# Kernel tuning notes

Hardware: AMD Instinct MI355X
Metric: run time of the kernel (lower is better)

Reference implementation:

```python
import jax, jax.numpy as jnp
import numpy as np

# dims
N, T, DIN = 256, 32, 2048      # batch, time, gpt output dim
H = 2048                        # MLP hidden
G, C, D = 2, 16, 256            # vq groups, codebook size, code dim
W, A = 5, 7                     # action window, action dim
WA = W * A                      # output_size
DEC_H = 512                     # vqvae decoder hidden
NT = N * T


def _mk(key, shape, scale=0.02):
    return jax.random.normal(key, shape, dtype=jnp.float32) * scale


def setup_inputs() -> dict:
    key = jax.random.key(0)
    ks = jax.random.split(key, 16)
    inp = {
        "x": jax.random.normal(ks[0], (N, T, DIN), dtype=jnp.float32),
        # bin1 MLP: DIN -> H -> H -> C
        "w11": _mk(ks[1], (DIN, H)), "b11": jnp.zeros((H,), jnp.float32),
        "w12": _mk(ks[2], (H, H)),   "b12": jnp.zeros((H,), jnp.float32),
        "w13": _mk(ks[3], (H, C)),   "b13": jnp.zeros((C,), jnp.float32),
        # bin2 MLP: DIN+C -> H -> C
        "w21": _mk(ks[4], (DIN + C, H)), "b21": jnp.zeros((H,), jnp.float32),
        "w22": _mk(ks[5], (H, C)),       "b22": jnp.zeros((C,), jnp.float32),
        # offset MLP: DIN -> H -> H -> G*C*WA
        "wo1": _mk(ks[6], (DIN, H)), "bo1": jnp.zeros((H,), jnp.float32),
        "wo2": _mk(ks[7], (H, H)),   "bo2": jnp.zeros((H,), jnp.float32),
        "wo3": _mk(ks[8], (H, G * C * WA)), "bo3": jnp.zeros((G * C * WA,), jnp.float32),
        # residual-VQ codebooks: (G, C, D)
        "codebook": _mk(ks[9], (G, C, D), scale=1.0),
        # frozen vqvae decoder: G*D -> DEC_H -> WA
        "wd1": _mk(ks[10], (G * D, DEC_H)), "bd1": jnp.zeros((DEC_H,), jnp.float32),
        "wd2": _mk(ks[11], (DEC_H, WA)),    "bd2": jnp.zeros((WA,), jnp.float32),
    }
    return inp


def reference(x, w11, b11, w12, b12, w13, b13, w21, b21, w22, b22,
              wo1, bo1, wo2, bo2, wo3, bo3, codebook, wd1, bd1, wd2, bd2):
    xf = x.reshape(NT, DIN)
    # bin1 logits
    h = jax.nn.relu(xf @ w11 + b11)
    h = jax.nn.relu(h @ w12 + b12)
    cbet_logits1 = h @ w13 + b13                       # (NT, C)
    # offsets
    o = jax.nn.relu(xf @ wo1 + bo1)
    o = jax.nn.relu(o @ wo2 + bo2)
    cbet_offsets = (o @ wo3 + bo3).reshape(NT, G, C, WA)
    # multinomial sampling (== categorical over softmax(logits))
    key = jax.random.key(42)
    k1, k2 = jax.random.split(key)
    s1 = jax.random.categorical(k1, cbet_logits1)      # (NT,)
    one_hot1 = jax.nn.one_hot(s1, C, dtype=xf.dtype)
    h2 = jax.nn.relu(jnp.concatenate([xf, one_hot1], axis=1) @ w21 + b21)
    cbet_logits2 = h2 @ w22 + b22                      # (NT, C)
    s2 = jax.random.categorical(k2, cbet_logits2)
    sampled_centers = jnp.stack([s1, s2], axis=1)      # (NT, G)
    # gather offsets at sampled codes, sum over groups
    nt_idx = jnp.arange(NT)[:, None]
    g_idx = jnp.arange(G)[None, :]
    sampled_offsets = cbet_offsets[nt_idx, g_idx, sampled_centers].sum(axis=1)  # (NT, WA)
    # vq codebook lookup + frozen decoder (detached in torch)
    centers = codebook[g_idx, sampled_centers]          # (NT, G, D)
    dec_in = jax.lax.stop_gradient(centers.reshape(NT, G * D))
    decoded = jax.nn.relu(dec_in @ wd1 + bd1) @ wd2 + bd2
    decoded = jax.lax.stop_gradient(decoded)            # (NT, WA)
    predicted = (decoded.reshape(NT, W, A) + sampled_offsets.reshape(NT, W, A))
    predicted_action = predicted.reshape(N, T, WA)
    return predicted_action, decoded, cbet_logits1, cbet_logits2, sampled_centers
```

## Files before the change

kernel.cpp:

```cpp
#include <hip/hip_runtime.h>
#include <cstdint>
#include <cstddef>

#define NT_   8192
#define DIN_  2048
#define H_    2048
#define C_    16
#define G_    2
#define D_    256
#define WA_   35
#define DECH_ 512
#define NPAD_ 1152

typedef _Float16 f16;
typedef _Float16 h4 __attribute__((ext_vector_type(4)));
typedef _Float16 h8 __attribute__((ext_vector_type(8)));
typedef float fx4 __attribute__((ext_vector_type(4)));

typedef __attribute__((address_space(1))) const void gvoid_t;
typedef __attribute__((address_space(3))) void lvoid_t;

__device__ __forceinline__ void gld16(const void* g, void* l) {
  __builtin_amdgcn_global_load_lds((gvoid_t*)(uintptr_t)g,
                                   (lvoid_t*)(uint32_t)(uintptr_t)l, 16, 0, 0);
}

__device__ __forceinline__ void barrier_() {
  asm volatile("" ::: "memory");
  __builtin_amdgcn_s_barrier();
  asm volatile("" ::: "memory");
}

template <int N>
__device__ __forceinline__ void waitvm() {
  if constexpr (N == 8)      asm volatile("s_waitcnt vmcnt(8)" ::: "memory");
  else if constexpr (N == 6) asm volatile("s_waitcnt vmcnt(6)" ::: "memory");
  else if constexpr (N == 2) asm volatile("s_waitcnt vmcnt(2)" ::: "memory");
  else                       asm volatile("s_waitcnt vmcnt(0)" ::: "memory");
}

#define MFMA_(d, a, b) d = __builtin_amdgcn_mfma_f32_16x16x32_f16(a, b, d, 0, 0, 0)

__host__ __device__ inline void tf2x32(uint32_t k0, uint32_t k1,
                                       uint32_t x0, uint32_t x1,
                                       uint32_t& o0, uint32_t& o1) {
  const uint32_t ks2 = k0 ^ k1 ^ 0x1BD11BDAu;
  uint32_t ks[3] = {k0, k1, ks2};
  x0 += ks[0]; x1 += ks[1];
  const uint32_t R0[4] = {13u, 15u, 26u, 6u};
  const uint32_t R1[4] = {17u, 29u, 16u, 24u};
#pragma unroll
  for (int g = 0; g < 5; ++g) {
    const uint32_t* R = (g & 1) ? R1 : R0;
#pragma unroll
    for (int r = 0; r < 4; ++r) {
      x0 += x1;
      x1 = (x1 << R[r]) | (x1 >> (32u - R[r]));
      x1 ^= x0;
    }
    x0 += ks[(g + 1) % 3];
    x1 += ks[(g + 2) % 3] + (uint32_t)(g + 1);
  }
  o0 = x0; o1 = x1;
}

__global__ __launch_bounds__(256) void xsplit_kernel(
    const float* __restrict__ x, f16* __restrict__ xh, f16* __restrict__ xl) {
  const size_t i = (size_t)blockIdx.x * 256 + threadIdx.x;
  const float4 v0 = *(const float4*)(x + i * 8);
  const float4 v1 = *(const float4*)(x + i * 8 + 4);
  float vv[8] = {v0.x, v0.y, v0.z, v0.w, v1.x, v1.y, v1.z, v1.w};
  h8 hh, ll;
#pragma unroll
  for (int k = 0; k < 8; ++k) {
    const f16 h = (f16)vv[k];
    hh[k] = h;
    ll[k] = (f16)(vv[k] - (float)h);
  }
  *(h8*)(xh + i * 8) = hh;
  *(h8*)(xl + i * 8) = ll;
}

enum { EPI_PAIR = 0, EPI_HI = 1, EPI_LOGIT = 2 };

template <int GATHER, int EPI>
__global__ __launch_bounds__(512, 2) void gemm256(
    const f16* __restrict__ Ah, const f16* __restrict__ Al,
    const f16* __restrict__ Bh, const f16* __restrict__ Bl,
    const float* __restrict__ bias,
    f16* __restrict__ Chi, f16* __restrict__ Clo,
    int M, int N, int K,
    const int* __restrict__ gidx, const float* __restrict__ growp, int gldw,
    const float* __restrict__ wlog, float* __restrict__ part) {
  extern __shared__ f16 lds[];
  constexpr int BS = 4 * 8192;

  const int tid  = threadIdx.x;
  const int wave = tid >> 6;
  const int lane = tid & 63;
  const int lr   = lane & 15;

  const int nb  = N >> 8;
  const int nwg = (int)gridDim.x;
  const int qq  = nwg >> 3;
  const int sw  = ((int)blockIdx.x & 7) * qq + ((int)blockIdx.x >> 3);
  const int by  = sw / nb, bx = sw % nb;
  const int m0  = by << 8, n0 = bx << 8;

  const int wm = (wave >> 2) * 128;
  const int wn = (wave & 3) * 64;

  fx4 acc[8][4];
#pragma unroll
  for (int i = 0; i < 8; ++i)
#pragma unroll
    for (int j = 0; j < 4; ++j) acc[i][j] = (fx4){0.f, 0.f, 0.f, 0.f};

  const int r_row = wave * 16 + (lane >> 2);
  const int r_g   = (lane & 3) ^ ((lane >> 3) & 3);
  const f16* gsrc[8];
  int gdst[8];
  {
    int nr = 0;
    auto AR = [&](const f16* P, int mn, int reg, int rb) {
      gsrc[nr] = P + (size_t)(mn + rb + r_row) * K + r_g * 8;
      gdst[nr] = reg * 8192 + rb * 32 + wave * 512;
      ++nr;
    };
    AR(Bh, n0, 2, 0); AR(Bh, n0, 2, 128);
    AR(Bl, n0, 3, 0); AR(Bl, n0, 3, 128);
    AR(Ah, m0, 0, 0); AR(Ah, m0, 0, 128);
    AR(Al, m0, 1, 0); AR(Al, m0, 1, 128);
  }

#pragma unroll
  for (int r = 0; r < 8; ++r) gld16(gsrc[r], lds + gdst[r]);
  waitvm<2>();
  barrier_();

  const int pg8 = ((lane >> 4) ^ ((lr >> 1) & 3)) * 8;
  const int KT  = K >> 5;

  for (int t = 0; t < KT; ++t) {
    f16* const sb  = lds + (t & 1) * BS;
    f16* const nsb = lds + ((t + 1) & 1) * BS;
    const int ktn = (t + 1 < KT ? t + 1 : t) * 32;

    const f16* sAh = sb;
    const f16* sAl = sb + 8192;
    const f16* sBh = sb + 16384;
    const f16* sBl = sb + 24576;

    h8 vbh[4], vbl[4], va[4];
#pragma unroll
    for (int j = 0; j < 4; ++j) {
      vbh[j] = *(const h8*)(sBh + (wn + j * 16 + lr) * 32 + pg8);
      vbl[j] = *(const h8*)(sBl + (wn + j * 16 + lr) * 32 + pg8);
    }
#pragma unroll
    for (int i = 0; i < 4; ++i)
      va[i] = *(const h8*)(sAh + (wm + i * 16 + lr) * 32 + pg8);
    gld16(gsrc[0] + ktn, nsb + gdst[0]);
    gld16(gsrc[1] + ktn, nsb + gdst[1]);
    gld16(gsrc[2] + ktn, nsb + gdst[2]);
    barrier_();
    asm volatile("s_waitcnt lgkmcnt(0)" ::: "memory");
    __builtin_amdgcn_sched_barrier(0);
    __builtin_amdgcn_s_setprio(1);
#pragma unroll
    for (int i = 0; i < 4; ++i)
#pragma unroll
      for (int j = 0; j < 4; ++j) MFMA_(acc[i][j], va[i], vbh[j]);
#pragma unroll
    for (int i = 0; i < 4; ++i)
#pragma unroll
      for (int j = 0; j < 4; ++j) MFMA_(acc[i][j], va[i], vbl[j]);
    __builtin_amdgcn_s_setprio(0);
    barrier_();
#pragma unroll
    for (int i = 0; i < 4; ++i)
      va[i] = *(const h8*)(sAh + (wm + 64 + i * 16 + lr) * 32 + pg8);
    gld16(gsrc[3] + ktn, nsb + gdst[3]);
    gld16(gsrc[4] + ktn, nsb + gdst[4]);
    gld16(gsrc[5] + ktn, nsb + gdst[5]);
    barrier_();
    asm volatile("s_waitcnt lgkmcnt(0)" ::: "memory");
    __builtin_amdgcn_sched_barrier(0);
    __builtin_amdgcn_s_setprio(1);
#pragma unroll
    for (int i = 0; i < 4; ++i)
#pragma unroll
      for (int j = 0; j < 4; ++j) MFMA_(acc[4 + i][j], va[i], vbh[j]);
#pragma unroll
    for (int i = 0; i < 4; ++i)
#pragma unroll
      for (int j = 0; j < 4; ++j) MFMA_(acc[4 + i][j], va[i], vbl[j]);
    __builtin_amdgcn_s_setprio(0);
    waitvm<6>();
    barrier_();
    {
      h8 vl0[4], vl1[4];
#pragma unroll
      for (int i = 0; i < 4; ++i) {
        vl0[i] = *(const h8*)(sAl + (wm + i * 16 + lr) * 32 + pg8);
        vl1[i] = *(const h8*)(sAl + (wm + 64 + i * 16 + lr) * 32 + pg8);
      }
      gld16(gsrc[6] + ktn, nsb + gdst[6]);
      gld16(gsrc[7] + ktn, nsb + gdst[7]);
      barrier_();
      asm volatile("s_waitcnt lgkmcnt(0)" ::: "memory");
      __builtin_amdgcn_sched_barrier(0);
      __builtin_amdgcn_s_setprio(1);
#pragma unroll
      for (int i = 0; i < 4; ++i)
#pragma unroll
        for (int j = 0; j < 4; ++j) {
          MFMA_(acc[i][j], vl0[i], vbh[j]);
          MFMA_(acc[4 + i][j], vl1[i], vbh[j]);
        }
      __builtin_amdgcn_s_setprio(0);
      waitvm<2>();
      barrier_();
    }
  }

  const int rq = (lane >> 4) * 4;
  if constexpr (EPI == EPI_LOGIT) {
#pragma unroll
    for (int mi = 0; mi < 8; ++mi) {
#pragma unroll
      for (int q = 0; q < 4; ++q) {
        const int row = m0 + wm + mi * 16 + rq + q;
        const float* gr = nullptr;
        if constexpr (GATHER) gr = growp + (size_t)gidx[row] * gldw;
#pragma unroll
        for (int j = 0; j < 4; ++j) {
          const int col = n0 + wn + j * 16 + lr;
          float v = acc[mi][j][q] + bias[col];
          if constexpr (GATHER) v += gr[col];
          acc[mi][j][q] = fmaxf(v, 0.f);
        }
      }
    }
    waitvm<0>();
    barrier_();
    float* psm = (float*)lds + wave * 2560;
    const int sidx = bx * 4 + (wave & 3);
    const int q_l = ((lr & 1) << 1) | ((lr >> 1) & 1);
    const int c_l = (((lr >> 2) & 1) << 1) | ((lr >> 3) & 1);
#pragma unroll
    for (int cc = 0; cc < 4; ++cc) {
      float wc[4][4];
#pragma unroll
      for (int j = 0; j < 4; ++j) {
        const float4 wv = *(const float4*)(wlog +
            (size_t)(n0 + wn + j * 16 + lr) * 16 + cc * 4);
        wc[j][0] = wv.x; wc[j][1] = wv.y; wc[j][2] = wv.z; wc[j][3] = wv.w;
      }
#pragma unroll
      for (int mi = 0; mi < 8; ++mi) {
        float A[16];
#pragma unroll
        for (int i = 0; i < 16; ++i) {
          float s = 0.f;
#pragma unroll
          for (int j = 0; j < 4; ++j)
            s = fmaf(acc[mi][j][i >> 2], wc[j][i & 3], s);
          A[i] = s;
        }
#pragma unroll
        for (int k = 0; k < 4; ++k) {
          const int L2 = 8 >> k;
          const bool b = (lr >> k) & 1;
          float An[8];
#pragma unroll
          for (int i = 0; i < L2; ++i) {
            const float keep = b ? A[i + L2] : A[i];
            const float send = b ? A[i] : A[i + L2];
            An[i] = keep + __shfl_xor(send, 1 << k);
          }
#pragma unroll
          for (int i = 0; i < L2; ++i) A[i] = An[i];
        }
        psm[mi * 320 + (rq + q_l) * 20 + cc * 4 + c_l] = A[0];
      }
    }
    asm volatile("s_waitcnt lgkmcnt(0)" ::: "memory");
#pragma unroll
    for (int mi = 0; mi < 8; ++mi) {
      const float4 o = *(const float4*)(psm + mi * 320 +
                                        (lane >> 2) * 20 + (lane & 3) * 4);
      float* pout = part + ((size_t)sidx * NT_ +
                            (m0 + wm + mi * 16 + (lane >> 2))) * 16 +
                    (lane & 3) * 4;
      *(float4*)pout = o;
    }
  } else {
#pragma unroll
    for (int mi = 0; mi < 8; ++mi) {
#pragma unroll
      for (int q = 0; q < 4; ++q) {
        const int row = m0 + wm + mi * 16 + rq + q;
#pragma unroll
        for (int j = 0; j < 4; ++j) {
          const int col = n0 + wn + j * 16 + lr;
          float v = fmaxf(acc[mi][j][q] + bias[col], 0.f);
          const f16 hh = (f16)v;
          Chi[(size_t)row * N + col] = hh;
          if constexpr (EPI == EPI_PAIR)
            Clo[(size_t)row * N + col] = (f16)(v - (float)hh);
        }
      }
    }
  }
}

__global__ __launch_bounds__(512, 2) void gemm256_1t(
    const f16* __restrict__ Ah, const f16* __restrict__ Bh,
    const float* __restrict__ bias, f16* __restrict__ Chi,
    int M, int N, int K) {
  extern __shared__ f16 lds[];
  constexpr int BS = 16384;

  const int tid  = threadIdx.x;
  const int wave = tid >> 6;
  const int lane = tid & 63;
  const int lr   = lane & 15;

  const int nb  = N >> 8;
  const int nwg = (int)gridDim.x;
  const int qq  = nwg >> 3;
  const int sw  = ((int)blockIdx.x & 7) * qq + ((int)blockIdx.x >> 3);
  const int by  = sw / nb, bx = sw % nb;
  const int m0  = by << 8, n0 = bx << 8;

  const int wm = (wave >> 2) * 128;
  const int wn = (wave & 3) * 64;

  fx4 acc[8][4];
#pragma unroll
  for (int i = 0; i < 8; ++i)
#pragma unroll
    for (int j = 0; j < 4; ++j) acc[i][j] = (fx4){0.f, 0.f, 0.f, 0.f};

  const int r_row = wave * 16 + (lane >> 2);
  const int r_g   = (lane & 3) ^ ((lane >> 3) & 3);
  const f16* gsrc[4];
  int gdst[4];
  {
    int nr = 0;
    auto AR = [&](const f16* P, int mn, int reg, int rb) {
      gsrc[nr] = P + (size_t)(mn + rb + r_row) * K + r_g * 8;
      gdst[nr] = reg * 8192 + rb * 32 + wave * 512;
      ++nr;
    };
    AR(Ah, m0, 0, 0); AR(Ah, m0, 0, 128);
    AR(Bh, n0, 1, 0); AR(Bh, n0, 1, 128);
  }

  const int KT  = K >> 5;
  const int pg8 = ((lane >> 4) ^ ((lr >> 1) & 3)) * 8;

#pragma unroll
  for (int r = 0; r < 4; ++r) gld16(gsrc[r], lds + gdst[r]);
#pragma unroll
  for (int r = 0; r < 4; ++r) gld16(gsrc[r] + 32, lds + BS + gdst[r]);

  int cur = 0, nn = 2;
  for (int t = 0; t < KT; ++t) {
    const int ktn = (t + 2 < KT ? t + 2 : KT - 1) * 32;
    f16* const nsb = lds + nn * BS;
#pragma unroll
    for (int r = 0; r < 4; ++r) gld16(gsrc[r] + ktn, nsb + gdst[r]);
    waitvm<8>();
    barrier_();

    const f16* sb = lds + cur * BS;
    h8 vb[4], va0[4], va1[4];
#pragma unroll
    for (int j = 0; j < 4; ++j)
      vb[j] = *(const h8*)(sb + 8192 + (wn + j * 16 + lr) * 32 + pg8);
#pragma unroll
    for (int i = 0; i < 4; ++i) {
      va0[i] = *(const h8*)(sb + (wm + i * 16 + lr) * 32 + pg8);
      va1[i] = *(const h8*)(sb + (wm + 64 + i * 16 + lr) * 32 + pg8);
    }
    asm volatile("s_waitcnt lgkmcnt(0)" ::: "memory");
    __builtin_amdgcn_sched_barrier(0);
    __builtin_amdgcn_s_setprio(1);
#pragma unroll
    for (int i = 0; i < 4; ++i)
#pragma unroll
      for (int j = 0; j < 4; ++j) {
        MFMA_(acc[i][j], va0[i], vb[j]);
        MFMA_(acc[4 + i][j], va1[i], vb[j]);
      }
    __builtin_amdgcn_s_setprio(0);
    barrier_();
    cur = (cur == 2) ? 0 : cur + 1;
    nn  = (nn == 2) ? 0 : nn + 1;
  }

  const int rq = (lane >> 4) * 4;
#pragma unroll
  for (int mi = 0; mi < 8; ++mi) {
#pragma unroll
    for (int q = 0; q < 4; ++q) {
      const int row = m0 + wm + mi * 16 + rq + q;
#pragma unroll
      for (int j = 0; j < 4; ++j) {
        const int col = n0 + wn + j * 16 + lr;
        Chi[(size_t)row * N + col] = (f16)fmaxf(acc[mi][j][q] + bias[col], 0.f);
      }
    }
  }
}

template <int RELU>
__global__ __launch_bounds__(256, 2) void gemm128(
    const f16* __restrict__ Ah, const f16* __restrict__ Bh,
    const float* __restrict__ bias, f16* __restrict__ Chi,
    int M, int N, int K) {
  __shared__ f16 lds[2 * 4096];
  f16* sAh = lds;
  f16* sBh = lds + 4096;

  const int tid  = threadIdx.x;
  const int wave = tid >> 6;
  const int lane = tid & 63;
  const int n0 = blockIdx.x * 128;
  const int m0 = blockIdx.y * 128;
  const int wm = (wave >> 1) * 64;
  const int wn = (wave & 1) * 64;
  const int lr = lane & 15;
  const int lk = (lane >> 4) * 8;

  fx4 acc[4][4];
#pragma unroll
  for (int i = 0; i < 4; ++i)
#pragma unroll
    for (int j = 0; j < 4; ++j) acc[i][j] = (fx4){0.f, 0.f, 0.f, 0.f};

  const int sb = wave * 2048 + (lane << 4);

  for (int kt = 0; kt < K; kt += 32) {
#pragma unroll
    for (int c = 0; c < 2; ++c) {
      const int boff = sb + c * 1024;
      const int row  = boff >> 6;
      const int col  = (boff & 63) >> 1;
      gld16(Bh + (size_t)(n0 + row) * K + kt + col, sBh + (wave * 2 + c) * 512);
      gld16(Ah + (size_t)(m0 + row) * K + kt + col, sAh + (wave * 2 + c) * 512);
    }
    __syncthreads();

    h8 ah[4], bh[4];
#pragma unroll
    for (int t = 0; t < 4; ++t) {
      ah[t] = *(const h8*)&sAh[(wm + t * 16 + lr) * 32 + lk];
      bh[t] = *(const h8*)&sBh[(wn + t * 16 + lr) * 32 + lk];
    }
#pragma unroll
    for (int i = 0; i < 4; ++i)
#pragma unroll
      for (int j = 0; j < 4; ++j) MFMA_(acc[i][j], ah[i], bh[j]);
    __syncthreads();
  }

  const int rq = (lane >> 4) * 4;
#pragma unroll
  for (int i = 0; i < 4; ++i) {
#pragma unroll
    for (int q = 0; q < 4; ++q) {
      const int row = m0 + wm + i * 16 + rq + q;
#pragma unroll
      for (int j = 0; j < 4; ++j) {
        const int col = n0 + wn + j * 16 + lr;
        float v = acc[i][j][q];
        if (bias) v += bias[col];
        if constexpr (RELU) v = fmaxf(v, 0.f);
        Chi[(size_t)row * N + col] = (f16)v;
      }
    }
  }
}

template <int SPLIT>
__global__ __launch_bounds__(256) void wtransT(
    const float* __restrict__ src, f16* __restrict__ hi, f16* __restrict__ lo,
    int K, int N, int Npad) {
  __shared__ float t[32][33];
  const int bn = blockIdx.x * 32;
  const int bk = blockIdx.y * 32;
  const int tx = threadIdx.x & 31, ty = threadIdx.x >> 5;
#pragma unroll
  for (int r = ty; r < 32; r += 8) {
    const float v = (bn + tx < N) ? src[(size_t)(bk + r) * N + bn + tx] : 0.f;
    t[tx][r] = v;
  }
  __syncthreads();
#pragma unroll
  for (int r = ty; r < 32; r += 8) {
    const float v = t[r][tx];
    const f16 hh = (f16)v;
    hi[(size_t)(bn + r) * K + bk + tx] = hh;
    if (SPLIT) lo[(size_t)(bn + r) * K + bk + tx] = (f16)(v - (float)hh);
  }
}

__global__ __launch_bounds__(256) void reduce_sample(
    const float* __restrict__ part, const float* __restrict__ bias,
    float* __restrict__ logits_out, int* __restrict__ s_out,
    float* __restrict__ centers_out, uint32_t ka, uint32_t kb, int which) {
  const int tid = threadIdx.x;
  const int c = tid & 15;
  const int m = blockIdx.x * 16 + (tid >> 4);
  float v = bias[c];
#pragma unroll 8
  for (int s = 0; s < 32; ++s) v += part[((size_t)s * NT_ + m) * 16 + c];
  logits_out[(size_t)m * C_ + c] = v;
  const uint32_t j = (uint32_t)(m * C_ + c);
  uint32_t o0, o1;
  tf2x32(ka, kb, 0u, j, o0, o1);
  const uint32_t bits = o0 ^ o1;
  float u = __uint_as_float((bits >> 9) | 0x3f800000u) - 1.0f;
  u = fmaxf(1.17549435e-38f, u);
  float z = -logf(-logf(u)) + v;
  int bi = c;
#pragma unroll
  for (int st = 1; st < 16; st <<= 1) {
    const float oz = __shfl_xor(z, st);
    const int   ob = __shfl_xor(bi, st);
    if (oz > z || (oz == z && ob < bi)) { z = oz; bi = ob; }
  }
  if (c == 0) {
    s_out[m] = bi;
    centers_out[(size_t)m * G_ + which] = (float)bi;
  }
}

__global__ void gather_dec_kernel(const float* __restrict__ codebook,
                                  const int* __restrict__ s1,
                                  const int* __restrict__ s2,
                                  f16* __restrict__ dec_in) {
  const int idx = blockIdx.x * blockDim.x + threadIdx.x;
  const int m = idx >> 9, d = idx & 511;
  const int g = d >> 8, dd = d & 255;
  const int s = g ? s2[m] : s1[m];
  dec_in[idx] = (f16)codebook[(size_t)(g * C_ + s) * D_ + dd];
}

__global__ __launch_bounds__(320) void final2(
    const f16* __restrict__ P,
    const float* __restrict__ bo3,
    const f16* __restrict__ dech,
    const float* __restrict__ wd2, const float* __restrict__ bd2,
    const int* __restrict__ s1, const int* __restrict__ s2,
    float* __restrict__ out_pred, float* __restrict__ out_dec) {
  __shared__ float drow[DECH_];
  const int m = blockIdx.x;
  for (int i = threadIdx.x; i < DECH_; i += 320)
    drow[i] = (float)dech[(size_t)m * DECH_ + i];
  __syncthreads();
  const int a1 = s1[m], a2 = s2[m];
  const int c = threadIdx.x >> 3, g = threadIdx.x & 7;
  float pdec = 0.f;
  if (c < WA_) {
    for (int i = 0; i < DECH_ / 8; ++i) {
      const int k = g * (DECH_ / 8) + i;
      pdec = fmaf(drow[k], wd2[(size_t)k * WA_ + c], pdec);
    }
  }
#pragma unroll
  for (int off = 1; off < 8; off <<= 1) pdec += __shfl_xor(pdec, off);
  if (c < WA_ && g == 0) {
    const float dec = pdec + bd2[c];
    const float soff = (float)P[(size_t)m * NPAD_ + a1 * WA_ + c]
                     + (float)P[(size_t)m * NPAD_ + C_ * WA_ + a2 * WA_ + c]
                     + bo3[a1 * WA_ + c] + bo3[C_ * WA_ + a2 * WA_ + c];
    out_dec[(size_t)m * WA_ + c] = dec;
    out_pred[(size_t)m * WA_ + c] = dec + soff;
  }
}

extern "C" void kernel_launch(void* const* d_in, const int* in_sizes, int n_in,
                              void* d_out, int out_size, void* d_ws, size_t ws_size,
                              hipStream_t stream) {
  const float* x    = (const float*)d_in[0];
  const float* w11  = (const float*)d_in[1];
  const float* b11  = (const float*)d_in[2];
  const float* w12  = (const float*)d_in[3];
  const float* b12  = (const float*)d_in[4];
  const float* w13  = (const float*)d_in[5];
  const float* b13  = (const float*)d_in[6];
  const float* w21  = (const float*)d_in[7];
  const float* b21  = (const float*)d_in[8];
  const float* w22  = (const float*)d_in[9];
  const float* b22  = (const float*)d_in[10];
  const float* wo1  = (const float*)d_in[11];
  const float* bo1  = (const float*)d_in[12];
  const float* wo2  = (const float*)d_in[13];
  const float* bo2  = (const float*)d_in[14];
  const float* wo3  = (const float*)d_in[15];
  const float* bo3  = (const float*)d_in[16];
  const float* cbk  = (const float*)d_in[17];
  const float* wd1  = (const float*)d_in[18];
  const float* bd1  = (const float*)d_in[19];
  const float* wd2  = (const float*)d_in[20];
  const float* bd2  = (const float*)d_in[21];

  float* out = (float*)d_out;
  float* out_pred = out;
  float* out_dec  = out + (size_t)NT_ * WA_;
  float* out_l1   = out + (size_t)2 * NT_ * WA_;
  float* out_l2   = out_l1 + (size_t)NT_ * C_;
  float* out_sc   = out_l2 + (size_t)NT_ * C_;

  const size_t AB = (size_t)NT_ * H_;
  f16*   Xh   = (f16*)d_ws;
  f16*   Xl   = Xh + AB;
  f16*   H1a  = Xl + AB;
  f16*   H1b  = H1a + AB;
  f16*   WH   = H1b + AB;
  f16*   WL   = WH + (size_t)H_ * H_;
  float* PART = (float*)(WL + (size_t)H_ * H_);
  int*   S1   = (int*)(PART + (size_t)32 * NT_ * C_);
  int*   S2   = S1 + NT_;

  f16* O1    = H1a;
  f16* O2    = H1b;
  f16* P     = Xh;
  f16* DECIN = Xl;
  f16* DECH  = Xl + (size_t)NT_ * DECH_;

  hipFuncSetAttribute(reinterpret_cast<const void*>(&gemm256<0,EPI_PAIR>),
                      hipFuncAttributeMaxDynamicSharedMemorySize, 131072);
  hipFuncSetAttribute(reinterpret_cast<const void*>(&gemm256<0,EPI_LOGIT>),
                      hipFuncAttributeMaxDynamicSharedMemorySize, 131072);
  hipFuncSetAttribute(reinterpret_cast<const void*>(&gemm256<1,EPI_LOGIT>),
                      hipFuncAttributeMaxDynamicSharedMemorySize, 131072);
  hipFuncSetAttribute(reinterpret_cast<const void*>(&gemm256_1t),
                      hipFuncAttributeMaxDynamicSharedMemorySize, 98304);

  uint32_t k1a, k1b, k2a, k2b;
  tf2x32(0u, 42u, 0u, 0u, k1a, k1b);
  tf2x32(0u, 42u, 0u, 1u, k2a, k2b);

  const dim3 b256(256), b512(512);
  const dim3 gW(H_ / 32, H_ / 32);
  const dim3 gWo3(NPAD_ / 32, H_ / 32);
  const dim3 gWd1(DECH_ / 32, DECH_ / 32);
  const dim3 gBig((NT_ / 256) * (H_ / 256));
  const dim3 gP(NPAD_ / 128, NT_ / 128);
  const dim3 gD(DECH_ / 128, NT_ / 128);

  xsplit_kernel<<<NT_ * H_ / (8 * 256), b256, 0, stream>>>(x, Xh, Xl);

  wtransT<1><<<gW, b256, 0, stream>>>(w11, WH, WL, H_, H_, H_);
  gemm256<0,EPI_PAIR><<<gBig, b512, 131072, stream>>>(
      Xh, Xl, WH, WL, b11, H1a, H1b, NT_, H_, DIN_,
      nullptr, nullptr, 0, nullptr, nullptr);
  wtransT<1><<<gW, b256, 0, stream>>>(w12, WH, WL, H_, H_, H_);
  gemm256<0,EPI_LOGIT><<<gBig, b512, 131072, stream>>>(
      H1a, H1b, WH, WL, b12, nullptr, nullptr, NT_, H_, H_,
      nullptr, nullptr, 0, w13, PART);
  reduce_sample<<<NT_ / 16, b256, 0, stream>>>(PART, b13, out_l1, S1, out_sc,
                                               k1a, k1b, 0);

  wtransT<1><<<gW, b256, 0, stream>>>(w21, WH, WL, H_, H_, H_);
  gemm256<1,EPI_LOGIT><<<gBig, b512, 131072, stream>>>(
      Xh, Xl, WH, WL, b21, nullptr, nullptr, NT_, H_, DIN_,
      S1, w21 + (size_t)DIN_ * H_, H_, w22, PART);
  reduce_sample<<<NT_ / 16, b256, 0, stream>>>(PART, b22, out_l2, S2, out_sc,
                                               k2a, k2b, 1);

  wtransT<0><<<gW, b256, 0, stream>>>(wo1, WH, nullptr, H_, H_, H_);
  gemm256_1t<<<gBig, b512, 98304, stream>>>(Xh, WH, bo1, O1, NT_, H_, DIN_);
  wtransT<0><<<gW, b256, 0, stream>>>(wo2, WH, nullptr, H_, H_, H_);
  gemm256_1t<<<gBig, b512, 98304, stream>>>(O1, WH, bo2, O2, NT_, H_, H_);
  wtransT<0><<<gWo3, b256, 0, stream>>>(wo3, WH, nullptr, H_, G_ * C_ * WA_, NPAD_);
  gemm128<0><<<gP, b256, 0, stream>>>(O2, WH, nullptr, P, NT_, NPAD_, H_);

  gather_dec_kernel<<<(NT_ * DECH_) / 256, b256, 0, stream>>>(cbk, S1, S2, DECIN);
  wtransT<0><<<gWd1, b256, 0, stream>>>(wd1, WH, nullptr, DECH_, DECH_, DECH_);
  gemm128<1><<<gD, b256, 0, stream>>>(DECIN, WH, bd1, DECH, NT_, DECH_, DECH_);

  final2<<<NT_, 320, 0, stream>>>(P, bo3, DECH, wd2, bd2, S1, S2,
                                  out_pred, out_dec);

  (void)in_sizes; (void)n_in; (void)out_size; (void)ws_size;
}
```

Before: 950.2 us.

## Switch GEMMs to 32x32x16 MFMA and unify small GEMMs on 256-tile kernel

Rewrites the split-precision first-layer GEMM and the single-precision offset/decoder GEMMs to use 32x32x16 MFMA instructions instead of 16x16x32. The split-precision GEMM is restructured into a double-buffered pipeline that interleaves the hi/lo loads with the three partial products. The 128-tile gemm128 kernel is dropped and the wo3 and decoder GEMMs now run on the 256-tile kernel, which needs NPAD raised to 1280 so it divides by 256. The larger MFMA shape is meant to cut LDS reads per flop and raise MFMA throughput. The cost is more padded work on the wo3 GEMM and fewer workgroups for the small GEMMs (64 blocks for the decoder).

```diff
diff --git a/kernel.cpp b/kernel.cpp
--- a/kernel.cpp
+++ b/kernel.cpp
@@ -10,12 +10,13 @@
 #define D_    256
 #define WA_   35
 #define DECH_ 512
-#define NPAD_ 1152
+#define NPAD_ 1280
 
 typedef _Float16 f16;
 typedef _Float16 h4 __attribute__((ext_vector_type(4)));
 typedef _Float16 h8 __attribute__((ext_vector_type(8)));
 typedef float fx4 __attribute__((ext_vector_type(4)));
+typedef float fx16 __attribute__((ext_vector_type(16)));
 
 typedef __attribute__((address_space(1))) const void gvoid_t;
 typedef __attribute__((address_space(3))) void lvoid_t;
@@ -35,11 +36,14 @@
 __device__ __forceinline__ void waitvm() {
   if constexpr (N == 8)      asm volatile("s_waitcnt vmcnt(8)" ::: "memory");
   else if constexpr (N == 6) asm volatile("s_waitcnt vmcnt(6)" ::: "memory");
+  else if constexpr (N == 5) asm volatile("s_waitcnt vmcnt(5)" ::: "memory");
+  else if constexpr (N == 4) asm volatile("s_waitcnt vmcnt(4)" ::: "memory");
   else if constexpr (N == 2) asm volatile("s_waitcnt vmcnt(2)" ::: "memory");
   else                       asm volatile("s_waitcnt vmcnt(0)" ::: "memory");
 }
 
-#define MFMA_(d, a, b) d = __builtin_amdgcn_mfma_f32_16x16x32_f16(a, b, d, 0, 0, 0)
+#define MFMA_(d, a, b)  d = __builtin_amdgcn_mfma_f32_16x16x32_f16(a, b, d, 0, 0, 0)
+#define MFMA32_(d, a, b) d = __builtin_amdgcn_mfma_f32_32x32x16_f16(a, b, d, 0, 0, 0)
 
 __host__ __device__ inline void tf2x32(uint32_t k0, uint32_t k1,
                                        uint32_t x0, uint32_t x1,
@@ -315,17 +319,20 @@
   }
 }
 
-__global__ __launch_bounds__(512, 2) void gemm256_1t(
-    const f16* __restrict__ Ah, const f16* __restrict__ Bh,
-    const float* __restrict__ bias, f16* __restrict__ Chi,
+__global__ __launch_bounds__(512, 2) void gemm256p32(
+    const f16* __restrict__ Ah, const f16* __restrict__ Al,
+    const f16* __restrict__ Bh, const f16* __restrict__ Bl,
+    const float* __restrict__ bias,
+    f16* __restrict__ Chi, f16* __restrict__ Clo,
     int M, int N, int K) {
   extern __shared__ f16 lds[];
-  constexpr int BS = 16384;
+  constexpr int BS = 4 * 8192;
 
   const int tid  = threadIdx.x;
   const int wave = tid >> 6;
   const int lane = tid & 63;
-  const int lr   = lane & 15;
+  const int cl   = lane & 31;
+  const int hs   = lane >> 5;
 
   const int nb  = N >> 8;
   const int nwg = (int)gridDim.x;
@@ -337,11 +344,184 @@
   const int wm = (wave >> 2) * 128;
   const int wn = (wave & 3) * 64;
 
-  fx4 acc[8][4];
-#pragma unroll
-  for (int i = 0; i < 8; ++i)
-#pragma unroll
-    for (int j = 0; j < 4; ++j) acc[i][j] = (fx4){0.f, 0.f, 0.f, 0.f};
+  fx16 acc[4][2];
+#pragma unroll
+  for (int f = 0; f < 4; ++f)
+#pragma unroll
+    for (int g = 0; g < 2; ++g)
+#pragma unroll
+      for (int r = 0; r < 16; ++r) acc[f][g][r] = 0.f;
+
+  const int r_row = wave * 16 + (lane >> 2);
+  const int r_g   = (lane & 3) ^ ((lane >> 3) & 3);
+  const f16* gsrc[8];
+  int gdst[8];
+  {
+    int nr = 0;
+    auto AR = [&](const f16* P, int mn, int reg, int rb) {
+      gsrc[nr] = P + (size_t)(mn + rb + r_row) * K + r_g * 8;
+      gdst[nr] = reg * 8192 + rb * 32 + wave * 512;
+      ++nr;
+    };
+    AR(Ah, m0, 0, 0); AR(Ah, m0, 0, 128);
+    AR(Bh, n0, 2, 0); AR(Bh, n0, 2, 128);
+    AR(Bl, n0, 3, 0); AR(Bl, n0, 3, 128);
+    AR(Al, m0, 1, 0); AR(Al, m0, 1, 128);
+  }
+
+#pragma unroll
+  for (int r = 0; r < 8; ++r) gld16(gsrc[r], lds + gdst[r]);
+  waitvm<4>();
+  barrier_();
+
+  const int rsw = (cl >> 1) & 3;
+  const int KT  = K >> 5;
+
+  for (int t = 0; t < KT; ++t) {
+    f16* const sb  = lds + (t & 1) * BS;
+    f16* const nsb = lds + ((t + 1) & 1) * BS;
+    const int ktn = (t + 1 < KT ? t + 1 : t) * 32;
+
+    const f16* sAh = sb;
+    const f16* sAl = sb + 8192;
+    const f16* sBh = sb + 16384;
+    const f16* sBl = sb + 24576;
+
+    const int g0 = (((0 * 2 + hs) ^ rsw) * 8);
+    const int g1 = (((1 * 2 + hs) ^ rsw) * 8);
+
+    h8 ah[4][2], bh[2][2];
+#pragma unroll
+    for (int f = 0; f < 4; ++f) {
+      const int row = wm + f * 32 + cl;
+      ah[f][0] = *(const h8*)(sAh + row * 32 + g0);
+      ah[f][1] = *(const h8*)(sAh + row * 32 + g1);
+    }
+#pragma unroll
+    for (int g = 0; g < 2; ++g) {
+      const int row = wn + g * 32 + cl;
+      bh[g][0] = *(const h8*)(sBh + row * 32 + g0);
+      bh[g][1] = *(const h8*)(sBh + row * 32 + g1);
+    }
+    gld16(gsrc[0] + ktn, nsb + gdst[0]);
+    gld16(gsrc[1] + ktn, nsb + gdst[1]);
+    gld16(gsrc[2] + ktn, nsb + gdst[2]);
+    barrier_();
+    asm volatile("s_waitcnt lgkmcnt(0)" ::: "memory");
+    __builtin_amdgcn_sched_barrier(0);
+    __builtin_amdgcn_s_setprio(1);
+#pragma unroll
+    for (int f = 0; f < 4; ++f)
+#pragma unroll
+      for (int g = 0; g < 2; ++g) {
+        MFMA32_(acc[f][g], ah[f][0], bh[g][0]);
+        MFMA32_(acc[f][g], ah[f][1], bh[g][1]);
+      }
+    __builtin_amdgcn_s_setprio(0);
+    waitvm<5>();
+    barrier_();
+    {
+      h8 bl[2][2];
+#pragma unroll
+      for (int g = 0; g < 2; ++g) {
+        const int row = wn + g * 32 + cl;
+        bl[g][0] = *(const h8*)(sBl + row * 32 + g0);
+        bl[g][1] = *(const h8*)(sBl + row * 32 + g1);
+      }
+      gld16(gsrc[3] + ktn, nsb + gdst[3]);
+      gld16(gsrc[4] + ktn, nsb + gdst[4]);
+      gld16(gsrc[5] + ktn, nsb + gdst[5]);
+      barrier_();
+      asm volatile("s_waitcnt lgkmcnt(0)" ::: "memory");
+      __builtin_amdgcn_sched_barrier(0);
+      __builtin_amdgcn_s_setprio(1);
+#pragma unroll
+      for (int f = 0; f < 4; ++f)
+#pragma unroll
+        for (int g = 0; g < 2; ++g) {
+          MFMA32_(acc[f][g], ah[f][0], bl[g][0]);
+          MFMA32_(acc[f][g], ah[f][1], bl[g][1]);
+        }
+      __builtin_amdgcn_s_setprio(0);
+      waitvm<6>();
+      barrier_();
+    }
+    {
+      h8 al[4][2];
+#pragma unroll
+      for (int f = 0; f < 4; ++f) {
+        const int row = wm + f * 32 + cl;
+        al[f][0] = *(const h8*)(sAl + row * 32 + g0);
+        al[f][1] = *(const h8*)(sAl + row * 32 + g1);
+      }
+      gld16(gsrc[6] + ktn, nsb + gdst[6]);
+      gld16(gsrc[7] + ktn, nsb + gdst[7]);
+      barrier_();
+      asm volatile("s_waitcnt lgkmcnt(0)" ::: "memory");
+      __builtin_amdgcn_sched_barrier(0);
+      __builtin_amdgcn_s_setprio(1);
+#pragma unroll
+      for (int f = 0; f < 4; ++f)
+#pragma unroll
+        for (int g = 0; g < 2; ++g) {
+          MFMA32_(acc[f][g], al[f][0], bh[g][0]);
+          MFMA32_(acc[f][g], al[f][1], bh[g][1]);
+        }
+      __builtin_amdgcn_s_setprio(0);
+      waitvm<4>();
+      barrier_();
+    }
+  }
+
+#pragma unroll
+  for (int f = 0; f < 4; ++f) {
+#pragma unroll
+    for (int g = 0; g < 2; ++g) {
+      const int col = n0 + wn + g * 32 + cl;
+      const float bb = bias[col];
+#pragma unroll
+      for (int r = 0; r < 16; ++r) {
+        const int row = m0 + wm + f * 32 + (r & 3) + 8 * (r >> 2) + 4 * hs;
+        const float v = fmaxf(acc[f][g][r] + bb, 0.f);
+        const f16 hh = (f16)v;
+        Chi[(size_t)row * N + col] = hh;
+        Clo[(size_t)row * N + col] = (f16)(v - (float)hh);
+      }
+    }
+  }
+}
+
+template <int RELU>
+__global__ __launch_bounds__(512, 2) void g1t32(
+    const f16* __restrict__ Ah, const f16* __restrict__ Bh,
+    const float* __restrict__ bias, f16* __restrict__ Chi,
+    int M, int N, int K) {
+  extern __shared__ f16 lds[];
+  constexpr int BS = 16384;
+
+  const int tid  = threadIdx.x;
+  const int wave = tid >> 6;
+  const int lane = tid & 63;
+  const int cl   = lane & 31;
+  const int hs   = lane >> 5;
+
+  const int nb  = N >> 8;
+  const int nwg = (int)gridDim.x;
+  const int qq  = nwg >> 3;
+  const int sw  = ((int)blockIdx.x & 7) * qq + ((int)blockIdx.x >> 3);
+  const int by  = sw / nb, bx = sw % nb;
+  const int m0  = by << 8, n0 = bx << 8;
+
+  const int wm = (wave >> 2) * 128;
+  const int wn = (wave & 3) * 64;
+
+  fx16 acc[4][2];
+#pragma unroll
+  for (int f = 0; f < 4; ++f)
+#pragma unroll
+    for (int g = 0; g < 2; ++g)
+#pragma unroll
+      for (int r = 0; r < 16; ++r) acc[f][g][r] = 0.f;
 
   const int r_row = wave * 16 + (lane >> 2);
   const int r_g   = (lane & 3) ^ ((lane >> 3) & 3);
@@ -359,7 +539,7 @@
   }
 
   const int KT  = K >> 5;
-  const int pg8 = ((lane >> 4) ^ ((lr >> 1) & 3)) * 8;
+  const int rsw = (cl >> 1) & 3;
 
 #pragma unroll
   for (int r = 0; r < 4; ++r) gld16(gsrc[r], lds + gdst[r]);
@@ -376,24 +556,30 @@
     barrier_();
 
     const f16* sb = lds + cur * BS;
-    h8 vb[4], va0[4], va1[4];
-#pragma unroll
-    for (int j = 0; j < 4; ++j)
-      vb[j] = *(const h8*)(sb + 8192 + (wn + j * 16 + lr) * 32 + pg8);
-#pragma unroll
-    for (int i = 0; i < 4; ++i) {
-      va0[i] = *(const h8*)(sb + (wm + i * 16 + lr) * 32 + pg8);
-      va1[i] = *(const h8*)(sb + (wm + 64 + i * 16 + lr) * 32 + pg8);
+    const int g0 = (((0 * 2 + hs) ^ rsw) * 8);
+    const int g1 = (((1 * 2 + hs) ^ rsw) * 8);
+    h8 a[4][2], b[2][2];
+#pragma unroll
+    for (int f = 0; f < 4; ++f) {
+      const int row = wm + f * 32 + cl;
+      a[f][0] = *(const h8*)(sb + row * 32 + g0);
+      a[f][1] = *(const h8*)(sb + row * 32 + g1);
+    }
+#pragma unroll
+    for (int g = 0; g < 2; ++g) {
+      const int row = wn + g * 32 + cl;
+      b[g][0] = *(const h8*)(sb + 8192 + row * 32 + g0);
+      b[g][1] = *(const h8*)(sb + 8192 + row * 32 + g1);
     }
     asm volatile("s_waitcnt lgkmcnt(0)" ::: "memory");
     __builtin_amdgcn_sched_barrier(0);
     __builtin_amdgcn_s_setprio(1);
 #pragma unroll
-    for (int i = 0; i < 4; ++i)
-#pragma unroll
-      for (int j = 0; j < 4; ++j) {
-        MFMA_(acc[i][j], va0[i], vb[j]);
-        MFMA_(acc[4 + i][j], va1[i], vb[j]);
+    for (int f = 0; f < 4; ++f)
+#pragma unroll
+      for (int g = 0; g < 2; ++g) {
+        MFMA32_(acc[f][g], a[f][0], b[g][0]);
+        MFMA32_(acc[f][g], a[f][1], b[g][1]);
       }
     __builtin_amdgcn_s_setprio(0);
     barrier_();
@@ -401,83 +587,16 @@
     nn  = (nn == 2) ? 0 : nn + 1;
   }
 
-  const int rq = (lane >> 4) * 4;
-#pragma unroll
-  for (int mi = 0; mi < 8; ++mi) {
-#pragma unroll
-    for (int q = 0; q < 4; ++q) {
-      const int row = m0 + wm + mi * 16 + rq + q;
-#pragma unroll
-      for (int j = 0; j < 4; ++j) {
-        const int col = n0 + wn + j * 16 + lr;
-        Chi[(size_t)row * N + col] = (f16)fmaxf(acc[mi][j][q] + bias[col], 0.f);
-      }
-    }
-  }
-}
-
-template <int RELU>
-__global__ __launch_bounds__(256, 2) void gemm128(
-    const f16* __restrict__ Ah, const f16* __restrict__ Bh,
-    const float* __restrict__ bias, f16* __restrict__ Chi,
-    int M, int N, int K) {
-  __shared__ f16 lds[2 * 4096];
-  f16* sAh = lds;
-  f16* sBh = lds + 4096;
-
-  const int tid  = threadIdx.x;
-  const int wave = tid >> 6;
-  const int lane = tid & 63;
-  const int n0 = blockIdx.x * 128;
-  const int m0 = blockIdx.y * 128;
-  const int wm = (wave >> 1) * 64;
-  const int wn = (wave & 1) * 64;
-  const int lr = lane & 15;
-  const int lk = (lane >> 4) * 8;
-
-  fx4 acc[4][4];
-#pragma unroll
-  for (int i = 0; i < 4; ++i)
-#pragma unroll
-    for (int j = 0; j < 4; ++j) acc[i][j] = (fx4){0.f, 0.f, 0.f, 0.f};
-
-  const int sb = wave * 2048 + (lane << 4);
-
-  for (int kt = 0; kt < K; kt += 32) {
-#pragma unroll
-    for (int c = 0; c < 2; ++c) {
-      const int boff = sb + c * 1024;
-      const int row  = boff >> 6;
-      const int col  = (boff & 63) >> 1;
-      gld16(Bh + (size_t)(n0 + row) * K + kt + col, sBh + (wave * 2 + c) * 512);
-      gld16(Ah + (size_t)(m0 + row) * K + kt + col, sAh + (wave * 2 + c) * 512);
-    }
-    __syncthreads();
-
-    h8 ah[4], bh[4];
-#pragma unroll
-    for (int t = 0; t < 4; ++t) {
-      ah[t] = *(const h8*)&sAh[(wm + t * 16 + lr) * 32 + lk];
-      bh[t] = *(const h8*)&sBh[(wn + t * 16 + lr) * 32 + lk];
-    }
-#pragma unroll
-    for (int i = 0; i < 4; ++i)
-#pragma unroll
-      for (int j = 0; j < 4; ++j) MFMA_(acc[i][j], ah[i], bh[j]);
-    __syncthreads();
-  }
-
-  const int rq = (lane >> 4) * 4;
-#pragma unroll
-  for (int i = 0; i < 4; ++i) {
-#pragma unroll
-    for (int q = 0; q < 4; ++q) {
-      const int row = m0 + wm + i * 16 + rq + q;
-#pragma unroll
-      for (int j = 0; j < 4; ++j) {
-        const int col = n0 + wn + j * 16 + lr;
-        float v = acc[i][j][q];
-        if (bias) v += bias[col];
+#pragma unroll
+  for (int f = 0; f < 4; ++f) {
+#pragma unroll
+    for (int g = 0; g < 2; ++g) {
+      const int col = n0 + wn + g * 32 + cl;
+      const float bb = bias ? bias[col] : 0.f;
+#pragma unroll
+      for (int r = 0; r < 16; ++r) {
+        const int row = m0 + wm + f * 32 + (r & 3) + 8 * (r >> 2) + 4 * hs;
+        float v = acc[f][g][r] + bb;
         if constexpr (RELU) v = fmaxf(v, 0.f);
         Chi[(size_t)row * N + col] = (f16)v;
       }
@@ -633,13 +752,15 @@
   f16* DECIN = Xl;
   f16* DECH  = Xl + (size_t)NT_ * DECH_;
 
-  hipFuncSetAttribute(reinterpret_cast<const void*>(&gemm256<0,EPI_PAIR>),
+  hipFuncSetAttribute(reinterpret_cast<const void*>(&gemm256p32),
                       hipFuncAttributeMaxDynamicSharedMemorySize, 131072);
   hipFuncSetAttribute(reinterpret_cast<const void*>(&gemm256<0,EPI_LOGIT>),
                       hipFuncAttributeMaxDynamicSharedMemorySize, 131072);
   hipFuncSetAttribute(reinterpret_cast<const void*>(&gemm256<1,EPI_LOGIT>),
                       hipFuncAttributeMaxDynamicSharedMemorySize, 131072);
-  hipFuncSetAttribute(reinterpret_cast<const void*>(&gemm256_1t),
+  hipFuncSetAttribute(reinterpret_cast<const void*>(&g1t32<0>),
+                      hipFuncAttributeMaxDynamicSharedMemorySize, 98304);
+  hipFuncSetAttribute(reinterpret_cast<const void*>(&g1t32<1>),
                       hipFuncAttributeMaxDynamicSharedMemorySize, 98304);
 
   uint32_t k1a, k1b, k2a, k2b;
@@ -651,15 +772,14 @@
   const dim3 gWo3(NPAD_ / 32, H_ / 32);
   const dim3 gWd1(DECH_ / 32, DECH_ / 32);
   const dim3 gBig((NT_ / 256) * (H_ / 256));
-  const dim3 gP(NPAD_ / 128, NT_ / 128);
-  const dim3 gD(DECH_ / 128, NT_ / 128);
+  const dim3 gP((NT_ / 256) * (NPAD_ / 256));
+  const dim3 gD((NT_ / 256) * (DECH_ / 256));
 
   xsplit_kernel<<<NT_ * H_ / (8 * 256), b256, 0, stream>>>(x, Xh, Xl);
 
   wtransT<1><<<gW, b256, 0, stream>>>(w11, WH, WL, H_, H_, H_);
-  gemm256<0,EPI_PAIR><<<gBig, b512, 131072, stream>>>(
-      Xh, Xl, WH, WL, b11, H1a, H1b, NT_, H_, DIN_,
-      nullptr, nullptr, 0, nullptr, nullptr);
+  gemm256p32<<<gBig, b512, 131072, stream>>>(
+      Xh, Xl, WH, WL, b11, H1a, H1b, NT_, H_, DIN_);
   wtransT<1><<<gW, b256, 0, stream>>>(w12, WH, WL, H_, H_, H_);
   gemm256<0,EPI_LOGIT><<<gBig, b512, 131072, stream>>>(
       H1a, H1b, WH, WL, b12, nullptr, nullptr, NT_, H_, H_,
@@ -675,15 +795,15 @@
                                                k2a, k2b, 1);
 
   wtransT<0><<<gW, b256, 0, stream>>>(wo1, WH, nullptr, H_, H_, H_);
-  gemm256_1t<<<gBig, b512, 98304, stream>>>(Xh, WH, bo1, O1, NT_, H_, DIN_);
+  g1t32<1><<<gBig, b512, 98304, stream>>>(Xh, WH, bo1, O1, NT_, H_, DIN_);
   wtransT<0><<<gW, b256, 0, stream>>>(wo2, WH, nullptr, H_, H_, H_);
-  gemm256_1t<<<gBig, b512, 98304, stream>>>(O1, WH, bo2, O2, NT_, H_, H_);
+  g1t32<1><<<gBig, b512, 98304, stream>>>(O1, WH, bo2, O2, NT_, H_, H_);
   wtransT<0><<<gWo3, b256, 0, stream>>>(wo3, WH, nullptr, H_, G_ * C_ * WA_, NPAD_);
-  gemm128<0><<<gP, b256, 0, stream>>>(O2, WH, nullptr, P, NT_, NPAD_, H_);
+  g1t32<0><<<gP, b512, 98304, stream>>>(O2, WH, nullptr, P, NT_, NPAD_, H_);
 
   gather_dec_kernel<<<(NT_ * DECH_) / 256, b256, 0, stream>>>(cbk, S1, S2, DECIN);
   wtransT<0><<<gWd1, b256, 0, stream>>>(wd1, WH, nullptr, DECH_, DECH_, DECH_);
-  gemm128<1><<<gD, b256, 0, stream>>>(DECIN, WH, bd1, DECH, NT_, DECH_, DECH_);
+  g1t32<1><<<gD, b512, 98304, stream>>>(DECIN, WH, bd1, DECH, NT_, DECH_, DECH_);
 
   final2<<<NT_, 320, 0, stream>>>(P, bo3, DECH, wd2, bd2, S1, S2,
                                   out_pred, out_dec);
```

Result: slower. 987.6 us (+3.9%).

## Drop intra-iteration barriers in split GEMM and reuse 256-tile GEMM for small GEMMs

Applied to the files above, without the earlier changes.

In the hi/lo split GEMM, both A half-tiles are now loaded up front and the first two MFMA phases are merged. This removes several workgroup barriers and explicit lgkmcnt waits per K-step, so LDS reads, async prefetches and MFMAs can overlap. The single-term 256 GEMM also loses its explicit lgkmcnt wait. It is templated on ReLU and now replaces the 128-tile GEMM for the offset-head output and the decoder hidden layer. NPAD is raised to 1280 so those shapes fit 256-wide tiles, at the cost of padding waste and far fewer workgroups for these small GEMMs.

```diff
diff --git a/kernel.cpp b/kernel.cpp
--- a/kernel.cpp
+++ b/kernel.cpp
@@ -10,7 +10,7 @@
 #define D_    256
 #define WA_   35
 #define DECH_ 512
-#define NPAD_ 1152
+#define NPAD_ 1280
 
 typedef _Float16 f16;
 typedef _Float16 h4 __attribute__((ext_vector_type(4)));
@@ -151,50 +151,40 @@
     const f16* sBh = sb + 16384;
     const f16* sBl = sb + 24576;
 
-    h8 vbh[4], vbl[4], va[4];
+    h8 vbh[4], vbl[4], va[4], va2[4];
 #pragma unroll
     for (int j = 0; j < 4; ++j) {
       vbh[j] = *(const h8*)(sBh + (wn + j * 16 + lr) * 32 + pg8);
       vbl[j] = *(const h8*)(sBl + (wn + j * 16 + lr) * 32 + pg8);
     }
 #pragma unroll
-    for (int i = 0; i < 4; ++i)
-      va[i] = *(const h8*)(sAh + (wm + i * 16 + lr) * 32 + pg8);
+    for (int i = 0; i < 4; ++i) {
+      va[i]  = *(const h8*)(sAh + (wm + i * 16 + lr) * 32 + pg8);
+      va2[i] = *(const h8*)(sAh + (wm + 64 + i * 16 + lr) * 32 + pg8);
+    }
     gld16(gsrc[0] + ktn, nsb + gdst[0]);
     gld16(gsrc[1] + ktn, nsb + gdst[1]);
     gld16(gsrc[2] + ktn, nsb + gdst[2]);
-    barrier_();
-    asm volatile("s_waitcnt lgkmcnt(0)" ::: "memory");
-    __builtin_amdgcn_sched_barrier(0);
-    __builtin_amdgcn_s_setprio(1);
-#pragma unroll
-    for (int i = 0; i < 4; ++i)
-#pragma unroll
-      for (int j = 0; j < 4; ++j) MFMA_(acc[i][j], va[i], vbh[j]);
-#pragma unroll
-    for (int i = 0; i < 4; ++i)
-#pragma unroll
-      for (int j = 0; j < 4; ++j) MFMA_(acc[i][j], va[i], vbl[j]);
-    __builtin_amdgcn_s_setprio(0);
-    barrier_();
-#pragma unroll
-    for (int i = 0; i < 4; ++i)
-      va[i] = *(const h8*)(sAh + (wm + 64 + i * 16 + lr) * 32 + pg8);
     gld16(gsrc[3] + ktn, nsb + gdst[3]);
     gld16(gsrc[4] + ktn, nsb + gdst[4]);
     gld16(gsrc[5] + ktn, nsb + gdst[5]);
-    barrier_();
-    asm volatile("s_waitcnt lgkmcnt(0)" ::: "memory");
-    __builtin_amdgcn_sched_barrier(0);
     __builtin_amdgcn_s_setprio(1);
 #pragma unroll
     for (int i = 0; i < 4; ++i)
 #pragma unroll
-      for (int j = 0; j < 4; ++j) MFMA_(acc[4 + i][j], va[i], vbh[j]);
+      for (int j = 0; j < 4; ++j) MFMA_(acc[i][j], va[i], vbh[j]);
 #pragma unroll
     for (int i = 0; i < 4; ++i)
 #pragma unroll
-      for (int j = 0; j < 4; ++j) MFMA_(acc[4 + i][j], va[i], vbl[j]);
+      for (int j = 0; j < 4; ++j) MFMA_(acc[i][j], va[i], vbl[j]);
+#pragma unroll
+    for (int i = 0; i < 4; ++i)
+#pragma unroll
+      for (int j = 0; j < 4; ++j) MFMA_(acc[4 + i][j], va2[i], vbh[j]);
+#pragma unroll
+    for (int i = 0; i < 4; ++i)
+#pragma unroll
+      for (int j = 0; j < 4; ++j) MFMA_(acc[4 + i][j], va2[i], vbl[j]);
     __builtin_amdgcn_s_setprio(0);
     waitvm<6>();
     barrier_();
@@ -207,9 +197,6 @@
       }
       gld16(gsrc[6] + ktn, nsb + gdst[6]);
       gld16(gsrc[7] + ktn, nsb + gdst[7]);
-      barrier_();
-      asm volatile("s_waitcnt lgkmcnt(0)" ::: "memory");
-      __builtin_amdgcn_sched_barrier(0);
       __builtin_amdgcn_s_setprio(1);
 #pragma unroll
       for (int i = 0; i < 4; ++i)
@@ -315,6 +302,7 @@
   }
 }
 
+template <int RELU>
 __global__ __launch_bounds__(512, 2) void gemm256_1t(
     const f16* __restrict__ Ah, const f16* __restrict__ Bh,
     const float* __restrict__ bias, f16* __restrict__ Chi,
@@ -385,8 +373,6 @@
       va0[i] = *(const h8*)(sb + (wm + i * 16 + lr) * 32 + pg8);
       va1[i] = *(const h8*)(sb + (wm + 64 + i * 16 + lr) * 32 + pg8);
     }
-    asm volatile("s_waitcnt lgkmcnt(0)" ::: "memory");
-    __builtin_amdgcn_sched_barrier(0);
     __builtin_amdgcn_s_setprio(1);
 #pragma unroll
     for (int i = 0; i < 4; ++i)
@@ -410,73 +396,7 @@
 #pragma unroll
       for (int j = 0; j < 4; ++j) {
         const int col = n0 + wn + j * 16 + lr;
-        Chi[(size_t)row * N + col] = (f16)fmaxf(acc[mi][j][q] + bias[col], 0.f);
-      }
-    }
-  }
-}
-
-template <int RELU>
-__global__ __launch_bounds__(256, 2) void gemm128(
-    const f16* __restrict__ Ah, const f16* __restrict__ Bh,
-    const float* __restrict__ bias, f16* __restrict__ Chi,
-    int M, int N, int K) {
-  __shared__ f16 lds[2 * 4096];
-  f16* sAh = lds;
-  f16* sBh = lds + 4096;
-
-  const int tid  = threadIdx.x;
-  const int wave = tid >> 6;
-  const int lane = tid & 63;
-  const int n0 = blockIdx.x * 128;
-  const int m0 = blockIdx.y * 128;
-  const int wm = (wave >> 1) * 64;
-  const int wn = (wave & 1) * 64;
-  const int lr = lane & 15;
-  const int lk = (lane >> 4) * 8;
-
-  fx4 acc[4][4];
-#pragma unroll
-  for (int i = 0; i < 4; ++i)
-#pragma unroll
-    for (int j = 0; j < 4; ++j) acc[i][j] = (fx4){0.f, 0.f, 0.f, 0.f};
-
-  const int sb = wave * 2048 + (lane << 4);
-
-  for (int kt = 0; kt < K; kt += 32) {
-#pragma unroll
-    for (int c = 0; c < 2; ++c) {
-      const int boff = sb + c * 1024;
-      const int row  = boff >> 6;
-      const int col  = (boff & 63) >> 1;
-      gld16(Bh + (size_t)(n0 + row) * K + kt + col, sBh + (wave * 2 + c) * 512);
-      gld16(Ah + (size_t)(m0 + row) * K + kt + col, sAh + (wave * 2 + c) * 512);
-    }
-    __syncthreads();
-
-    h8 ah[4], bh[4];
-#pragma unroll
-    for (int t = 0; t < 4; ++t) {
-      ah[t] = *(const h8*)&sAh[(wm + t * 16 + lr) * 32 + lk];
-      bh[t] = *(const h8*)&sBh[(wn + t * 16 + lr) * 32 + lk];
-    }
-#pragma unroll
-    for (int i = 0; i < 4; ++i)
-#pragma unroll
-      for (int j = 0; j < 4; ++j) MFMA_(acc[i][j], ah[i], bh[j]);
-    __syncthreads();
-  }
-
-  const int rq = (lane >> 4) * 4;
-#pragma unroll
-  for (int i = 0; i < 4; ++i) {
-#pragma unroll
-    for (int q = 0; q < 4; ++q) {
-      const int row = m0 + wm + i * 16 + rq + q;
-#pragma unroll
-      for (int j = 0; j < 4; ++j) {
-        const int col = n0 + wn + j * 16 + lr;
-        float v = acc[i][j][q];
+        float v = acc[mi][j][q];
         if (bias) v += bias[col];
         if constexpr (RELU) v = fmaxf(v, 0.f);
         Chi[(size_t)row * N + col] = (f16)v;
@@ -639,7 +559,9 @@
                       hipFuncAttributeMaxDynamicSharedMemorySize, 131072);
   hipFuncSetAttribute(reinterpret_cast<const void*>(&gemm256<1,EPI_LOGIT>),
                       hipFuncAttributeMaxDynamicSharedMemorySize, 131072);
-  hipFuncSetAttribute(reinterpret_cast<const void*>(&gemm256_1t),
+  hipFuncSetAttribute(reinterpret_cast<const void*>(&gemm256_1t<0>),
+                      hipFuncAttributeMaxDynamicSharedMemorySize, 98304);
+  hipFuncSetAttribute(reinterpret_cast<const void*>(&gemm256_1t<1>),
                       hipFuncAttributeMaxDynamicSharedMemorySize, 98304);
 
   uint32_t k1a, k1b, k2a, k2b;
@@ -651,8 +573,8 @@
   const dim3 gWo3(NPAD_ / 32, H_ / 32);
   const dim3 gWd1(DECH_ / 32, DECH_ / 32);
   const dim3 gBig((NT_ / 256) * (H_ / 256));
-  const dim3 gP(NPAD_ / 128, NT_ / 128);
-  const dim3 gD(DECH_ / 128, NT_ / 128);
+  const dim3 gP((NT_ / 256) * (NPAD_ / 256));
+  const dim3 gD((NT_ / 256) * (DECH_ / 256));
 
   xsplit_kernel<<<NT_ * H_ / (8 * 256), b256, 0, stream>>>(x, Xh, Xl);
 
@@ -675,15 +597,15 @@
                                                k2a, k2b, 1);
 
   wtransT<0><<<gW, b256, 0, stream>>>(wo1, WH, nullptr, H_, H_, H_);
-  gemm256_1t<<<gBig, b512, 98304, stream>>>(Xh, WH, bo1, O1, NT_, H_, DIN_);
+  gemm256_1t<1><<<gBig, b512, 98304, stream>>>(Xh, WH, bo1, O1, NT_, H_, DIN_);
   wtransT<0><<<gW, b256, 0, stream>>>(wo2, WH, nullptr, H_, H_, H_);
-  gemm256_1t<<<gBig, b512, 98304, stream>>>(O1, WH, bo2, O2, NT_, H_, H_);
+  gemm256_1t<1><<<gBig, b512, 98304, stream>>>(O1, WH, bo2, O2, NT_, H_, H_);
   wtransT<0><<<gWo3, b256, 0, stream>>>(wo3, WH, nullptr, H_, G_ * C_ * WA_, NPAD_);
-  gemm128<0><<<gP, b256, 0, stream>>>(O2, WH, nullptr, P, NT_, NPAD_, H_);
+  gemm256_1t<0><<<gP, b512, 98304, stream>>>(O2, WH, nullptr, P, NT_, NPAD_, H_);
 
   gather_dec_kernel<<<(NT_ * DECH_) / 256, b256, 0, stream>>>(cbk, S1, S2, DECIN);
   wtransT<0><<<gWd1, b256, 0, stream>>>(wd1, WH, nullptr, DECH_, DECH_, DECH_);
-  gemm128<1><<<gD, b256, 0, stream>>>(DECIN, WH, bd1, DECH, NT_, DECH_, DECH_);
+  gemm256_1t<1><<<gD, b512, 98304, stream>>>(DECIN, WH, bd1, DECH, NT_, DECH_, DECH_);
 
   final2<<<NT_, 320, 0, stream>>>(P, bo3, DECH, wd2, bd2, S1, S2,
                                   out_pred, out_dec);
```

Result: no change. 967.0 us (+1.8%).
